# Kernel tuning notes

Measured on AMD Instinct MI355X. Metric: run time of the kernel, lower is better.

The kernel has to match this reference:

```python
import jax, jax.numpy as jnp
import numpy as np

GROUPS = 32
EPS = 1e-5


def setup_inputs() -> dict:
    key = jax.random.key(0)
    ks = jax.random.split(key, 7)
    B, C, H, W = 16, 512, 32, 32
    return {
        "x": jax.random.normal(ks[0], (B, C, H, W), jnp.float32),
        "norm_w": jax.random.uniform(ks[1], (C,), jnp.float32, 0.5, 1.5),
        "norm_b": jax.random.normal(ks[2], (C,), jnp.float32) * 0.1,
        "qkv_w": jax.random.normal(ks[3], (3 * C, C), jnp.float32) * (C ** -0.5),
        "qkv_b": jax.random.normal(ks[4], (3 * C,), jnp.float32) * 0.01,
        "proj_w": jax.random.normal(ks[5], (C, C), jnp.float32) * (C ** -0.5),
        "proj_b": jax.random.normal(ks[6], (C,), jnp.float32) * 0.01,
        "num_heads": 8,
    }


def _group_norm(x, w, b):
    # x: (B, C, T); GroupNorm over (C//G, T) per group, per-channel affine
    B, C, T = x.shape
    xg = x.reshape(B, GROUPS, C // GROUPS, T)
    mean = jnp.mean(xg, axis=(2, 3), keepdims=True)
    var = jnp.var(xg, axis=(2, 3), keepdims=True)
    xn = ((xg - mean) * jax.lax.rsqrt(var + EPS)).reshape(B, C, T)
    return xn * w[None, :, None] + b[None, :, None]


def reference(x, norm_w, norm_b, qkv_w, qkv_b, proj_w, proj_b, num_heads):
    B, C, H, W = x.shape
    T = H * W
    xf = x.reshape(B, C, T)
    # qkv conv1x1: (B, 3C, T)
    qkv = jnp.einsum('oc,bct->bot', qkv_w, _group_norm(xf, norm_w, norm_b)) \
        + qkv_b[None, :, None]
    # split heads: (B*H, 3*hd, T) then chunk on channel dim
    BH = B * num_heads
    qkv = qkv.reshape(BH, 3 * C // num_heads, T)
    q, k, v = jnp.split(qkv, 3, axis=1)  # each (BH, hd, T)
    hd = C // num_heads
    scale = hd ** -0.25
    # scores (BH, T, T), softmax in fp32 then cast back (matches torch)
    scores = jnp.einsum('bct,bcs->bts', q * scale, k * scale)
    w = jax.nn.softmax(scores.astype(jnp.float32), axis=-1).astype(scores.dtype)
    h = jnp.einsum('bts,bcs->bct', w, v)  # (BH, hd, T)
    h = h.reshape(B, C, T)
    h = jnp.einsum('oc,bct->bot', proj_w, h) + proj_b[None, :, None]
    return (h + xf).reshape(B, C, H, W)
```

## Files before the change

kernel.cpp:

```cpp
#include <hip/hip_runtime.h>

typedef unsigned short u16;
typedef unsigned int u32;
typedef __bf16 bf16x8 __attribute__((ext_vector_type(8)));
typedef float f32x4 __attribute__((ext_vector_type(4)));
typedef float f32x16 __attribute__((ext_vector_type(16)));

#define SCALE_QK 0.35355339059327373f
#define LOG2E 1.4426950408889634f

__device__ __forceinline__ u16 f2bf(float f) {
  u32 u = __float_as_uint(f);
  u += 0x7FFFu + ((u >> 16) & 1u);
  return (u16)(u >> 16);
}

__device__ __forceinline__ void gload16(const u16* g, u16* l) {
  __builtin_amdgcn_global_load_lds((const __attribute__((address_space(1))) void*)g,
                                   (__attribute__((address_space(3))) void*)l, 16, 0, 0);
}

__device__ __forceinline__ int rswz(int r) { return (r & 7) ^ ((r >> 3) & 3); }

__global__ __launch_bounds__(256) void k_convert(const float* __restrict__ src,
                                                 u16* __restrict__ dst, int n4) {
  int i = blockIdx.x * 256 + threadIdx.x;
  if (i >= n4) return;
  float4 v = ((const float4*)src)[i];
  u32 lo = (u32)f2bf(v.x) | ((u32)f2bf(v.y) << 16);
  u32 hi = (u32)f2bf(v.z) | ((u32)f2bf(v.w) << 16);
  ((uint2*)dst)[i] = make_uint2(lo, hi);
}

__global__ __launch_bounds__(256) void k_groupnorm(const float* __restrict__ x,
                                                   const float* __restrict__ nw,
                                                   const float* __restrict__ nb,
                                                   u16* __restrict__ gnt) {
  const int b = blockIdx.x >> 5;
  const int g = blockIdx.x & 31;
  const int tid = threadIdx.x;
  const float* xg = x + ((size_t)b * 512 + g * 16) * 1024;

  float s = 0.f, ss = 0.f;
#pragma unroll
  for (int it = 0; it < 16; ++it) {
    float4 v = ((const float4*)xg)[tid + it * 256];
    s += v.x + v.y + v.z + v.w;
    ss += v.x * v.x + v.y * v.y + v.z * v.z + v.w * v.w;
  }
#pragma unroll
  for (int off = 32; off >= 1; off >>= 1) {
    s += __shfl_xor(s, off);
    ss += __shfl_xor(ss, off);
  }
  __shared__ float red[8];
  const int wid = tid >> 6, lane = tid & 63;
  if (lane == 0) { red[wid] = s; red[4 + wid] = ss; }
  __syncthreads();
  const float mean = (red[0] + red[1] + red[2] + red[3]) * (1.f / 16384.f);
  const float ex2 = (red[4] + red[5] + red[6] + red[7]) * (1.f / 16384.f);
  const float rstd = rsqrtf(ex2 - mean * mean + 1e-5f);

  const int ci = tid & 15, tt = tid >> 4;
  const int c = g * 16 + ci;
  const float wc = nw[c] * rstd;
  const float bc = nb[c] - mean * wc;
  const float* xc = xg + (size_t)ci * 1024;
  u16* dst = gnt + (size_t)b * 1024 * 512 + c;
#pragma unroll 8
  for (int t = tt; t < 1024; t += 16) {
    dst[(size_t)t * 512] = f2bf(xc[t] * wc + bc);
  }
}

template <int MODE>
__global__ __launch_bounds__(512) void k_gemm(const u16* __restrict__ A,
                                              const u16* __restrict__ Bw,
                                              const float* __restrict__ bias,
                                              u16* __restrict__ Qb, u16* __restrict__ Kb,
                                              u16* __restrict__ Vb,
                                              const float* __restrict__ xres,
                                              float* __restrict__ out) {
  __shared__ u16 As[2][128][64];
  __shared__ u16 Bs[2][128][64];
  const int tid = threadIdx.x;
  const int lane = tid & 63, wid = tid >> 6;
  const int wr = wid >> 1, wc = wid & 1;
  const int fid = blockIdx.x;
  const int m0 = (fid & 127) * 128;
  const int n0 = (fid >> 7) * 128;
  const int l15 = lane & 15, l4 = lane >> 4;
  const f32x4 fzero = {0.f, 0.f, 0.f, 0.f};

  f32x4 acc[2][4];
#pragma unroll
  for (int i = 0; i < 2; ++i)
#pragma unroll
    for (int j = 0; j < 4; ++j) acc[i][j] = fzero;

  const int lrow = (tid & 63) >> 3;
  const int lchunk = tid & 7;

  auto stage = [&](int bi, int kt) {
#pragma unroll
    for (int rd = 0; rd < 2; ++rd) {
      const int rbase = wid * 8 + rd * 64;
      const int r = rbase + lrow;
      const int q = lchunk ^ (r & 7);
      gload16(A + ((size_t)(m0 + r) * 512 + kt * 64 + q * 8), &As[bi][rbase][0]);
      gload16(Bw + ((size_t)(n0 + r) * 512 + kt * 64 + q * 8), &Bs[bi][rbase][0]);
    }
  };

  stage(0, 0);
  stage(1, 1);

  for (int kt = 0; kt < 8; ++kt) {
    if (kt < 7) {
      asm volatile("s_waitcnt vmcnt(4)" ::: "memory");
    } else {
      asm volatile("s_waitcnt vmcnt(0)" ::: "memory");
    }
    __builtin_amdgcn_s_barrier();
    const int buf = kt & 1;
#pragma unroll
    for (int ks = 0; ks < 2; ++ks) {
      bf16x8 af[2], bfr[4];
#pragma unroll
      for (int mi = 0; mi < 2; ++mi) {
        const int row = wr * 32 + mi * 16 + l15;
        af[mi] = *(const bf16x8*)&As[buf][row][(((ks << 2) + l4) ^ (row & 7)) << 3];
      }
#pragma unroll
      for (int ni = 0; ni < 4; ++ni) {
        const int row = wc * 64 + ni * 16 + l15;
        bfr[ni] = *(const bf16x8*)&Bs[buf][row][(((ks << 2) + l4) ^ (row & 7)) << 3];
      }
#pragma unroll
      for (int mi = 0; mi < 2; ++mi)
#pragma unroll
        for (int ni = 0; ni < 4; ++ni)
          acc[mi][ni] = __builtin_amdgcn_mfma_f32_16x16x32_bf16(af[mi], bfr[ni], acc[mi][ni], 0, 0, 0);
    }
    asm volatile("s_waitcnt lgkmcnt(0)" ::: "memory");
    __builtin_amdgcn_sched_barrier(0);
    __builtin_amdgcn_s_barrier();
    if (kt < 6) stage(buf, kt + 2);
  }

#pragma unroll
  for (int ni = 0; ni < 4; ++ni) {
    const int o = n0 + wc * 64 + ni * 16 + l15;
    const float bo = bias[o];
    if (MODE == 0) {
      const int h = o / 192;
      const int jo = o - h * 192;
      const int typ = jo >> 6;
      const int ci = jo & 63;
#pragma unroll
      for (int mi = 0; mi < 2; ++mi) {
        const int mrow = m0 + wr * 32 + mi * 16 + l4 * 4;
        const int b = mrow >> 10, t0 = mrow & 1023;
#pragma unroll
        for (int jj = 0; jj < 4; ++jj) {
          const float v = acc[mi][ni][jj] + bo;
          const int t = t0 + jj;
          if (typ == 0)
            Qb[(((size_t)(b * 8 + h) * 1024 + t) << 6) + ci] = f2bf(v * (SCALE_QK * LOG2E));
          else if (typ == 1)
            Kb[(((size_t)(b * 8 + h) * 1024 + t) << 6) + ci] = f2bf(v * SCALE_QK);
          else
            Vb[(((size_t)(b * 8 + h) * 64 + ci) << 10) + t] = f2bf(v);
        }
      }
    } else {
#pragma unroll
      for (int mi = 0; mi < 2; ++mi) {
        const int mrow = m0 + wr * 32 + mi * 16 + l4 * 4;
        const int b = mrow >> 10, t0 = mrow & 1023;
        const size_t base = ((size_t)b * 512 + o) * 1024 + t0;
        const float4 xr = *(const float4*)(xres + base);
        float4 ov;
        ov.x = acc[mi][ni][0] + bo + xr.x;
        ov.y = acc[mi][ni][1] + bo + xr.y;
        ov.z = acc[mi][ni][2] + bo + xr.z;
        ov.w = acc[mi][ni][3] + bo + xr.w;
        *(float4*)(out + base) = ov;
      }
    }
  }
}

__global__ __launch_bounds__(256) void k_attn(const u16* __restrict__ Qb,
                                              const u16* __restrict__ Kb,
                                              const u16* __restrict__ Vb,
                                              u16* __restrict__ ht) {
  __shared__ u16 Ks[2][64][64];
  __shared__ u16 Vs[2][64][64];
  const int tid = threadIdx.x;
  const int lane = tid & 63, wid = tid >> 6;
  const int l31 = lane & 31, hi = lane >> 5;
  const int fid = blockIdx.x;
  const int bh = fid & 127, qt = fid >> 7;
  const int b = bh >> 3, head = bh & 7;
  const int lrow = lane >> 3, lchunk = lane & 7;
  const int rsw = rswz(l31);

  bf16x8 qf[4];
  {
    const u16* qp = Qb + (((size_t)bh * 1024 + qt * 128 + wid * 32 + l31) << 6) + hi * 8;
#pragma unroll
    for (int kc = 0; kc < 4; ++kc) qf[kc] = *(const bf16x8*)(qp + kc * 16);
  }

  bf16x8 onesf;
#pragma unroll
  for (int i = 0; i < 8; ++i) onesf[i] = (l31 == 0) ? (__bf16)1.0f : (__bf16)0.0f;

  f32x16 oacc[2], osum;
#pragma unroll
  for (int r = 0; r < 16; ++r) { oacc[0][r] = 0.f; oacc[1][r] = 0.f; osum[r] = 0.f; }

  auto stageKV = [&](int bi, int st) {
    const int s0 = st * 64;
#pragma unroll
    for (int rd = 0; rd < 2; ++rd) {
      const int rbase = wid * 8 + rd * 32;
      const int r = rbase + lrow;
      const int q = lchunk ^ rswz(r);
      gload16(Kb + (((size_t)bh * 1024 + s0 + r) << 6) + q * 8, &Ks[bi][rbase][0]);
      gload16(Vb + (((size_t)bh * 64 + r) << 10) + s0 + q * 8, &Vs[bi][rbase][0]);
    }
  };

  stageKV(0, 0);
  stageKV(1, 1);

  for (int st = 0; st < 16; ++st) {
    if (st < 15) {
      asm volatile("s_waitcnt vmcnt(4)" ::: "memory");
    } else {
      asm volatile("s_waitcnt vmcnt(0)" ::: "memory");
    }
    __builtin_amdgcn_s_barrier();
    const int buf = st & 1;

#pragma unroll
    for (int cb = 0; cb < 2; ++cb) {
      f32x16 sacc;
#pragma unroll
      for (int r = 0; r < 16; ++r) sacc[r] = 0.f;
      __builtin_amdgcn_s_setprio(1);
#pragma unroll
      for (int kc = 0; kc < 4; ++kc) {
        const int r = cb * 32 + l31;
        const bf16x8 kb = *(const bf16x8*)&Ks[buf][r][((((kc << 1) | hi)) ^ rsw) << 3];
        sacc = __builtin_amdgcn_mfma_f32_32x32x16_bf16(kb, qf[kc], sacc, 0, 0, 0);
      }
      __builtin_amdgcn_s_setprio(0);
      float p[16];
#pragma unroll
      for (int r = 0; r < 16; ++r)
        asm("v_exp_f32 %0, %1" : "=v"(p[r]) : "v"(sacc[r]));

#pragma unroll
      for (int ksl = 0; ksl < 2; ++ksl) {
        u32 X0, X1, Y0, Y1;
        asm("v_cvt_pk_bf16_f32 %0, %1, %2" : "=v"(X0) : "v"(p[8 * ksl + 0]), "v"(p[8 * ksl + 1]));
        asm("v_cvt_pk_bf16_f32 %0, %1, %2" : "=v"(X1) : "v"(p[8 * ksl + 2]), "v"(p[8 * ksl + 3]));
        asm("v_cvt_pk_bf16_f32 %0, %1, %2" : "=v"(Y0) : "v"(p[8 * ksl + 4]), "v"(p[8 * ksl + 5]));
        asm("v_cvt_pk_bf16_f32 %0, %1, %2" : "=v"(Y1) : "v"(p[8 * ksl + 6]), "v"(p[8 * ksl + 7]));
        asm volatile("v_permlane32_swap_b32 %0, %1" : "+v"(X0), "+v"(Y0));
        asm volatile("v_permlane32_swap_b32 %0, %1" : "+v"(X1), "+v"(Y1));
        union { u32 w[4]; bf16x8 v; } pa;
        pa.w[0] = X0; pa.w[1] = X1; pa.w[2] = Y0; pa.w[3] = Y1;
        const int ks = cb * 2 + ksl;
        __builtin_amdgcn_s_setprio(1);
#pragma unroll
        for (int db = 0; db < 2; ++db) {
          const int r = db * 32 + l31;
          const bf16x8 vb = *(const bf16x8*)&Vs[buf][r][((((ks << 1) | hi)) ^ rsw) << 3];
          oacc[db] = __builtin_amdgcn_mfma_f32_32x32x16_bf16(pa.v, vb, oacc[db], 0, 0, 0);
        }
        osum = __builtin_amdgcn_mfma_f32_32x32x16_bf16(pa.v, onesf, osum, 0, 0, 0);
        __builtin_amdgcn_s_setprio(0);
      }
    }

    asm volatile("s_waitcnt lgkmcnt(0)" ::: "memory");
    __builtin_amdgcn_sched_barrier(0);
    __builtin_amdgcn_s_barrier();
    if (st < 14) stageKV(buf, st + 2);
  }

  float inv[16];
#pragma unroll
  for (int r = 0; r < 16; ++r) {
    const float ls = __shfl(osum[r], lane & 32);
    inv[r] = 1.f / ls;
  }
#pragma unroll
  for (int db = 0; db < 2; ++db) {
#pragma unroll
    for (int r = 0; r < 16; ++r) {
      const int t = qt * 128 + wid * 32 + (r & 3) + 8 * (r >> 2) + 4 * hi;
      const int cg = head * 64 + db * 32 + l31;
      ht[((size_t)b * 1024 + t) * 512 + cg] = f2bf(oacc[db][r] * inv[r]);
    }
  }
}

extern "C" void kernel_launch(void* const* d_in, const int* in_sizes, int n_in,
                              void* d_out, int out_size, void* d_ws, size_t ws_size,
                              hipStream_t stream) {
  const float* x = (const float*)d_in[0];
  const float* norm_w = (const float*)d_in[1];
  const float* norm_b = (const float*)d_in[2];
  const float* qkv_w = (const float*)d_in[3];
  const float* qkv_b = (const float*)d_in[4];
  const float* proj_w = (const float*)d_in[5];
  const float* proj_b = (const float*)d_in[6];
  float* out = (float*)d_out;

  char* ws = (char*)d_ws;
  u16* qkvw = (u16*)(ws + 0);
  u16* projw = (u16*)(ws + 1572864);
  u16* gnt = (u16*)(ws + 2097152);
  u16* Qb = (u16*)(ws + 18874368);
  u16* Kb = (u16*)(ws + 35651584);
  u16* Vb = (u16*)(ws + 52428800);
  u16* ht = (u16*)(ws + 69206016);

  k_convert<<<768, 256, 0, stream>>>(qkv_w, qkvw, 196608);
  k_convert<<<256, 256, 0, stream>>>(proj_w, projw, 65536);
  k_groupnorm<<<512, 256, 0, stream>>>(x, norm_w, norm_b, gnt);
  k_gemm<0><<<1536, 512, 0, stream>>>(gnt, qkvw, qkv_b, Qb, Kb, Vb, nullptr, nullptr);
  k_attn<<<1024, 256, 0, stream>>>(Qb, Kb, Vb, ht);
  k_gemm<1><<<512, 512, 0, stream>>>(ht, projw, proj_b, nullptr, nullptr, nullptr, x, out);
}
```

Measured before the change: 154.5 us.

## Use 32x32 MFMA tiles in GEMMs and two query tiles per attention wave

```diff
diff --git a/kernel.cpp b/kernel.cpp
--- a/kernel.cpp
+++ b/kernel.cpp
@@ -74,7 +74,7 @@
 }
 
 template <int MODE>
-__global__ __launch_bounds__(512) void k_gemm(const u16* __restrict__ A,
+__global__ __launch_bounds__(256) void k_gemm(const u16* __restrict__ A,
                                               const u16* __restrict__ Bw,
                                               const float* __restrict__ bias,
                                               u16* __restrict__ Qb, u16* __restrict__ Kb,
@@ -85,30 +85,32 @@
   __shared__ u16 Bs[2][128][64];
   const int tid = threadIdx.x;
   const int lane = tid & 63, wid = tid >> 6;
-  const int wr = wid >> 1, wc = wid & 1;
+  const int wm = wid >> 1, wn = wid & 1;
   const int fid = blockIdx.x;
   const int m0 = (fid & 127) * 128;
   const int n0 = (fid >> 7) * 128;
-  const int l15 = lane & 15, l4 = lane >> 4;
-  const f32x4 fzero = {0.f, 0.f, 0.f, 0.f};
-
-  f32x4 acc[2][4];
+  const int l31 = lane & 31, hi = lane >> 5;
+  const int rsw = rswz(l31);
+
+  f32x16 acc[2][2];
 #pragma unroll
   for (int i = 0; i < 2; ++i)
 #pragma unroll
-    for (int j = 0; j < 4; ++j) acc[i][j] = fzero;
-
-  const int lrow = (tid & 63) >> 3;
-  const int lchunk = tid & 7;
+    for (int j = 0; j < 2; ++j)
+#pragma unroll
+      for (int r = 0; r < 16; ++r) acc[i][j][r] = 0.f;
+
+  const int lr8 = lane >> 3, lc8 = lane & 7;
 
   auto stage = [&](int bi, int kt) {
-#pragma unroll
-    for (int rd = 0; rd < 2; ++rd) {
-      const int rbase = wid * 8 + rd * 64;
-      const int r = rbase + lrow;
-      const int q = lchunk ^ (r & 7);
-      gload16(A + ((size_t)(m0 + r) * 512 + kt * 64 + q * 8), &As[bi][rbase][0]);
-      gload16(Bw + ((size_t)(n0 + r) * 512 + kt * 64 + q * 8), &Bs[bi][rbase][0]);
+    u16* ab = &As[bi][0][0] + wid * 512;
+    u16* bb = &Bs[bi][0][0] + wid * 512;
+#pragma unroll
+    for (int i = 0; i < 4; ++i) {
+      const int r = wid * 8 + i * 32 + lr8;
+      const int c8 = lc8 ^ rswz(r);
+      gload16(A + ((size_t)(m0 + r) * 512 + kt * 64 + c8 * 8), ab + i * 2048);
+      gload16(Bw + ((size_t)(n0 + r) * 512 + kt * 64 + c8 * 8), bb + i * 2048);
     }
   };
 
@@ -117,30 +119,31 @@
 
   for (int kt = 0; kt < 8; ++kt) {
     if (kt < 7) {
-      asm volatile("s_waitcnt vmcnt(4)" ::: "memory");
+      asm volatile("s_waitcnt vmcnt(8)" ::: "memory");
     } else {
       asm volatile("s_waitcnt vmcnt(0)" ::: "memory");
     }
     __builtin_amdgcn_s_barrier();
     const int buf = kt & 1;
 #pragma unroll
-    for (int ks = 0; ks < 2; ++ks) {
-      bf16x8 af[2], bfr[4];
+    for (int kc = 0; kc < 4; ++kc) {
+      const int ch = kc * 2 + hi;
+      bf16x8 af[2], bfv[2];
 #pragma unroll
       for (int mi = 0; mi < 2; ++mi) {
-        const int row = wr * 32 + mi * 16 + l15;
-        af[mi] = *(const bf16x8*)&As[buf][row][(((ks << 2) + l4) ^ (row & 7)) << 3];
-      }
-#pragma unroll
-      for (int ni = 0; ni < 4; ++ni) {
-        const int row = wc * 64 + ni * 16 + l15;
-        bfr[ni] = *(const bf16x8*)&Bs[buf][row][(((ks << 2) + l4) ^ (row & 7)) << 3];
+        const int row = wm * 64 + mi * 32 + l31;
+        af[mi] = *(const bf16x8*)&As[buf][row][(ch ^ rsw) << 3];
+      }
+#pragma unroll
+      for (int ni = 0; ni < 2; ++ni) {
+        const int row = wn * 64 + ni * 32 + l31;
+        bfv[ni] = *(const bf16x8*)&Bs[buf][row][(ch ^ rsw) << 3];
       }
 #pragma unroll
       for (int mi = 0; mi < 2; ++mi)
 #pragma unroll
-        for (int ni = 0; ni < 4; ++ni)
-          acc[mi][ni] = __builtin_amdgcn_mfma_f32_16x16x32_bf16(af[mi], bfr[ni], acc[mi][ni], 0, 0, 0);
+        for (int ni = 0; ni < 2; ++ni)
+          acc[mi][ni] = __builtin_amdgcn_mfma_f32_32x32x16_bf16(af[mi], bfv[ni], acc[mi][ni], 0, 0, 0);
     }
     asm volatile("s_waitcnt lgkmcnt(0)" ::: "memory");
     __builtin_amdgcn_sched_barrier(0);
@@ -148,44 +151,50 @@
     if (kt < 6) stage(buf, kt + 2);
   }
 
-#pragma unroll
-  for (int ni = 0; ni < 4; ++ni) {
-    const int o = n0 + wc * 64 + ni * 16 + l15;
+  const int b = m0 >> 10;
+  const int t0b = m0 & 1023;
+#pragma unroll
+  for (int ni = 0; ni < 2; ++ni) {
+    const int o = n0 + wn * 64 + ni * 32 + l31;
     const float bo = bias[o];
     if (MODE == 0) {
       const int h = o / 192;
       const int jo = o - h * 192;
       const int typ = jo >> 6;
       const int ci = jo & 63;
+      const size_t qkbase = ((size_t)(b * 8 + h) * 1024) * 64 + ci;
+      const size_t vbase = ((size_t)(b * 8 + h) * 64 + ci) * 1024;
 #pragma unroll
       for (int mi = 0; mi < 2; ++mi) {
-        const int mrow = m0 + wr * 32 + mi * 16 + l4 * 4;
-        const int b = mrow >> 10, t0 = mrow & 1023;
-#pragma unroll
-        for (int jj = 0; jj < 4; ++jj) {
-          const float v = acc[mi][ni][jj] + bo;
-          const int t = t0 + jj;
+        const int t0m = t0b + wm * 64 + mi * 32;
+#pragma unroll
+        for (int r = 0; r < 16; ++r) {
+          const int t = t0m + (r & 3) + 8 * (r >> 2) + 4 * hi;
+          const float v = acc[mi][ni][r] + bo;
           if (typ == 0)
-            Qb[(((size_t)(b * 8 + h) * 1024 + t) << 6) + ci] = f2bf(v * (SCALE_QK * LOG2E));
+            Qb[qkbase + (size_t)t * 64] = f2bf(v * (SCALE_QK * LOG2E));
           else if (typ == 1)
-            Kb[(((size_t)(b * 8 + h) * 1024 + t) << 6) + ci] = f2bf(v * SCALE_QK);
+            Kb[qkbase + (size_t)t * 64] = f2bf(v * SCALE_QK);
           else
-            Vb[(((size_t)(b * 8 + h) * 64 + ci) << 10) + t] = f2bf(v);
+            Vb[vbase + t] = f2bf(v);
         }
       }
     } else {
+      const size_t obase = ((size_t)b * 512 + o) * 1024;
 #pragma unroll
       for (int mi = 0; mi < 2; ++mi) {
-        const int mrow = m0 + wr * 32 + mi * 16 + l4 * 4;
-        const int b = mrow >> 10, t0 = mrow & 1023;
-        const size_t base = ((size_t)b * 512 + o) * 1024 + t0;
-        const float4 xr = *(const float4*)(xres + base);
-        float4 ov;
-        ov.x = acc[mi][ni][0] + bo + xr.x;
-        ov.y = acc[mi][ni][1] + bo + xr.y;
-        ov.z = acc[mi][ni][2] + bo + xr.z;
-        ov.w = acc[mi][ni][3] + bo + xr.w;
-        *(float4*)(out + base) = ov;
+        const int t0m = t0b + wm * 64 + mi * 32;
+#pragma unroll
+        for (int rq = 0; rq < 4; ++rq) {
+          const int t = t0m + 8 * rq + 4 * hi;
+          const float4 xr = *(const float4*)(xres + obase + t);
+          float4 ov;
+          ov.x = acc[mi][ni][rq * 4 + 0] + bo + xr.x;
+          ov.y = acc[mi][ni][rq * 4 + 1] + bo + xr.y;
+          ov.z = acc[mi][ni][rq * 4 + 2] + bo + xr.z;
+          ov.w = acc[mi][ni][rq * 4 + 3] + bo + xr.w;
+          *(float4*)(out + obase + t) = ov;
+        }
       }
     }
   }
@@ -206,20 +215,26 @@
   const int lrow = lane >> 3, lchunk = lane & 7;
   const int rsw = rswz(l31);
 
-  bf16x8 qf[4];
+  bf16x8 qf0[4], qf1[4];
   {
-    const u16* qp = Qb + (((size_t)bh * 1024 + qt * 128 + wid * 32 + l31) << 6) + hi * 8;
-#pragma unroll
-    for (int kc = 0; kc < 4; ++kc) qf[kc] = *(const bf16x8*)(qp + kc * 16);
+    const u16* qp0 = Qb + (((size_t)bh * 1024 + qt * 256 + wid * 64 + l31) << 6) + hi * 8;
+    const u16* qp1 = qp0 + (32 << 6);
+#pragma unroll
+    for (int kc = 0; kc < 4; ++kc) {
+      qf0[kc] = *(const bf16x8*)(qp0 + kc * 16);
+      qf1[kc] = *(const bf16x8*)(qp1 + kc * 16);
+    }
   }
 
   bf16x8 onesf;
 #pragma unroll
   for (int i = 0; i < 8; ++i) onesf[i] = (l31 == 0) ? (__bf16)1.0f : (__bf16)0.0f;
 
-  f32x16 oacc[2], osum;
-#pragma unroll
-  for (int r = 0; r < 16; ++r) { oacc[0][r] = 0.f; oacc[1][r] = 0.f; osum[r] = 0.f; }
+  f32x16 oacc[2][2], osum[2];
+#pragma unroll
+  for (int g = 0; g < 2; ++g)
+#pragma unroll
+    for (int r = 0; r < 16; ++r) { oacc[g][0][r] = 0.f; oacc[g][1][r] = 0.f; osum[g][r] = 0.f; }
 
   auto stageKV = [&](int bi, int st) {
     const int s0 = st * 64;
@@ -247,42 +262,54 @@
 
 #pragma unroll
     for (int cb = 0; cb < 2; ++cb) {
-      f32x16 sacc;
-#pragma unroll
-      for (int r = 0; r < 16; ++r) sacc[r] = 0.f;
+      f32x16 sacc0, sacc1;
+#pragma unroll
+      for (int r = 0; r < 16; ++r) { sacc0[r] = 0.f; sacc1[r] = 0.f; }
       __builtin_amdgcn_s_setprio(1);
 #pragma unroll
       for (int kc = 0; kc < 4; ++kc) {
         const int r = cb * 32 + l31;
         const bf16x8 kb = *(const bf16x8*)&Ks[buf][r][((((kc << 1) | hi)) ^ rsw) << 3];
-        sacc = __builtin_amdgcn_mfma_f32_32x32x16_bf16(kb, qf[kc], sacc, 0, 0, 0);
+        sacc0 = __builtin_amdgcn_mfma_f32_32x32x16_bf16(kb, qf0[kc], sacc0, 0, 0, 0);
+        sacc1 = __builtin_amdgcn_mfma_f32_32x32x16_bf16(kb, qf1[kc], sacc1, 0, 0, 0);
       }
       __builtin_amdgcn_s_setprio(0);
-      float p[16];
-#pragma unroll
-      for (int r = 0; r < 16; ++r)
-        asm("v_exp_f32 %0, %1" : "=v"(p[r]) : "v"(sacc[r]));
+      float p0[16], p1[16];
+#pragma unroll
+      for (int r = 0; r < 16; ++r) {
+        asm("v_exp_f32 %0, %1" : "=v"(p0[r]) : "v"(sacc0[r]));
+        asm("v_exp_f32 %0, %1" : "=v"(p1[r]) : "v"(sacc1[r]));
+      }
 
 #pragma unroll
       for (int ksl = 0; ksl < 2; ++ksl) {
-        u32 X0, X1, Y0, Y1;
-        asm("v_cvt_pk_bf16_f32 %0, %1, %2" : "=v"(X0) : "v"(p[8 * ksl + 0]), "v"(p[8 * ksl + 1]));
-        asm("v_cvt_pk_bf16_f32 %0, %1, %2" : "=v"(X1) : "v"(p[8 * ksl + 2]), "v"(p[8 * ksl + 3]));
-        asm("v_cvt_pk_bf16_f32 %0, %1, %2" : "=v"(Y0) : "v"(p[8 * ksl + 4]), "v"(p[8 * ksl + 5]));
-        asm("v_cvt_pk_bf16_f32 %0, %1, %2" : "=v"(Y1) : "v"(p[8 * ksl + 6]), "v"(p[8 * ksl + 7]));
-        asm volatile("v_permlane32_swap_b32 %0, %1" : "+v"(X0), "+v"(Y0));
-        asm volatile("v_permlane32_swap_b32 %0, %1" : "+v"(X1), "+v"(Y1));
-        union { u32 w[4]; bf16x8 v; } pa;
-        pa.w[0] = X0; pa.w[1] = X1; pa.w[2] = Y0; pa.w[3] = Y1;
+        u32 A0, A1, B0, B1, C0, C1, D0, D1;
+        asm("v_cvt_pk_bf16_f32 %0, %1, %2" : "=v"(A0) : "v"(p0[8 * ksl + 0]), "v"(p0[8 * ksl + 1]));
+        asm("v_cvt_pk_bf16_f32 %0, %1, %2" : "=v"(A1) : "v"(p0[8 * ksl + 2]), "v"(p0[8 * ksl + 3]));
+        asm("v_cvt_pk_bf16_f32 %0, %1, %2" : "=v"(B0) : "v"(p0[8 * ksl + 4]), "v"(p0[8 * ksl + 5]));
+        asm("v_cvt_pk_bf16_f32 %0, %1, %2" : "=v"(B1) : "v"(p0[8 * ksl + 6]), "v"(p0[8 * ksl + 7]));
+        asm volatile("v_permlane32_swap_b32 %0, %1" : "+v"(A0), "+v"(B0));
+        asm volatile("v_permlane32_swap_b32 %0, %1" : "+v"(A1), "+v"(B1));
+        asm("v_cvt_pk_bf16_f32 %0, %1, %2" : "=v"(C0) : "v"(p1[8 * ksl + 0]), "v"(p1[8 * ksl + 1]));
+        asm("v_cvt_pk_bf16_f32 %0, %1, %2" : "=v"(C1) : "v"(p1[8 * ksl + 2]), "v"(p1[8 * ksl + 3]));
+        asm("v_cvt_pk_bf16_f32 %0, %1, %2" : "=v"(D0) : "v"(p1[8 * ksl + 4]), "v"(p1[8 * ksl + 5]));
+        asm("v_cvt_pk_bf16_f32 %0, %1, %2" : "=v"(D1) : "v"(p1[8 * ksl + 6]), "v"(p1[8 * ksl + 7]));
+        asm volatile("v_permlane32_swap_b32 %0, %1" : "+v"(C0), "+v"(D0));
+        asm volatile("v_permlane32_swap_b32 %0, %1" : "+v"(C1), "+v"(D1));
+        union { u32 w[4]; bf16x8 v; } pa0, pa1;
+        pa0.w[0] = A0; pa0.w[1] = A1; pa0.w[2] = B0; pa0.w[3] = B1;
+        pa1.w[0] = C0; pa1.w[1] = C1; pa1.w[2] = D0; pa1.w[3] = D1;
         const int ks = cb * 2 + ksl;
         __builtin_amdgcn_s_setprio(1);
 #pragma unroll
         for (int db = 0; db < 2; ++db) {
           const int r = db * 32 + l31;
           const bf16x8 vb = *(const bf16x8*)&Vs[buf][r][((((ks << 1) | hi)) ^ rsw) << 3];
-          oacc[db] = __builtin_amdgcn_mfma_f32_32x32x16_bf16(pa.v, vb, oacc[db], 0, 0, 0);
+          oacc[0][db] = __builtin_amdgcn_mfma_f32_32x32x16_bf16(pa0.v, vb, oacc[0][db], 0, 0, 0);
+          oacc[1][db] = __builtin_amdgcn_mfma_f32_32x32x16_bf16(pa1.v, vb, oacc[1][db], 0, 0, 0);
         }
-        osum = __builtin_amdgcn_mfma_f32_32x32x16_bf16(pa.v, onesf, osum, 0, 0, 0);
+        osum[0] = __builtin_amdgcn_mfma_f32_32x32x16_bf16(pa0.v, onesf, osum[0], 0, 0, 0);
+        osum[1] = __builtin_amdgcn_mfma_f32_32x32x16_bf16(pa1.v, onesf, osum[1], 0, 0, 0);
         __builtin_amdgcn_s_setprio(0);
       }
     }
@@ -293,19 +320,23 @@
     if (st < 14) stageKV(buf, st + 2);
   }
 
-  float inv[16];
-#pragma unroll
-  for (int r = 0; r < 16; ++r) {
-    const float ls = __shfl(osum[r], lane & 32);
-    inv[r] = 1.f / ls;
-  }
-#pragma unroll
-  for (int db = 0; db < 2; ++db) {
+#pragma unroll
+  for (int g = 0; g < 2; ++g) {
+    float inv[16];
 #pragma unroll
     for (int r = 0; r < 16; ++r) {
-      const int t = qt * 128 + wid * 32 + (r & 3) + 8 * (r >> 2) + 4 * hi;
-      const int cg = head * 64 + db * 32 + l31;
-      ht[((size_t)b * 1024 + t) * 512 + cg] = f2bf(oacc[db][r] * inv[r]);
+      const float ls = __shfl(osum[g][r], lane & 32);
+      inv[r] = 1.f / ls;
+    }
+    const int tg = qt * 256 + wid * 64 + g * 32;
+#pragma unroll
+    for (int db = 0; db < 2; ++db) {
+#pragma unroll
+      for (int r = 0; r < 16; ++r) {
+        const int t = tg + (r & 3) + 8 * (r >> 2) + 4 * hi;
+        const int cg = head * 64 + db * 32 + l31;
+        ht[((size_t)b * 1024 + t) * 512 + cg] = f2bf(oacc[g][db][r] * inv[r]);
+      }
     }
   }
 }
@@ -334,7 +365,7 @@
   k_convert<<<768, 256, 0, stream>>>(qkv_w, qkvw, 196608);
   k_convert<<<256, 256, 0, stream>>>(proj_w, projw, 65536);
   k_groupnorm<<<512, 256, 0, stream>>>(x, norm_w, norm_b, gnt);
-  k_gemm<0><<<1536, 512, 0, stream>>>(gnt, qkvw, qkv_b, Qb, Kb, Vb, nullptr, nullptr);
-  k_attn<<<1024, 256, 0, stream>>>(Qb, Kb, Vb, ht);
-  k_gemm<1><<<512, 512, 0, stream>>>(ht, projw, proj_b, nullptr, nullptr, nullptr, x, out);
-}
+  k_gemm<0><<<1536, 256, 0, stream>>>(gnt, qkvw, qkv_b, Qb, Kb, Vb, nullptr, nullptr);
+  k_attn<<<512, 256, 0, stream>>>(Qb, Kb, Vb, ht);
+  k_gemm<1><<<512, 256, 0, stream>>>(ht, projw, proj_b, nullptr, nullptr, nullptr, x, out);
+}
```

After: 158.4 us. +2.5%, slower.

## Process two query tiles per wave in attention to reuse K/V fragments

Applied to the files above, without the earlier changes.

```diff
diff --git a/kernel.cpp b/kernel.cpp
--- a/kernel.cpp
+++ b/kernel.cpp
@@ -191,7 +191,7 @@
   }
 }
 
-__global__ __launch_bounds__(256) void k_attn(const u16* __restrict__ Qb,
+__global__ __launch_bounds__(128) void k_attn(const u16* __restrict__ Qb,
                                               const u16* __restrict__ Kb,
                                               const u16* __restrict__ Vb,
                                               u16* __restrict__ ht) {
@@ -206,26 +206,32 @@
   const int lrow = lane >> 3, lchunk = lane & 7;
   const int rsw = rswz(l31);
 
-  bf16x8 qf[4];
+  bf16x8 qf0[4], qf1[4];
   {
-    const u16* qp = Qb + (((size_t)bh * 1024 + qt * 128 + wid * 32 + l31) << 6) + hi * 8;
-#pragma unroll
-    for (int kc = 0; kc < 4; ++kc) qf[kc] = *(const bf16x8*)(qp + kc * 16);
+    const u16* qp0 = Qb + (((size_t)bh * 1024 + qt * 128 + wid * 64 + l31) << 6) + hi * 8;
+    const u16* qp1 = qp0 + (32 << 6);
+#pragma unroll
+    for (int kc = 0; kc < 4; ++kc) {
+      qf0[kc] = *(const bf16x8*)(qp0 + kc * 16);
+      qf1[kc] = *(const bf16x8*)(qp1 + kc * 16);
+    }
   }
 
   bf16x8 onesf;
 #pragma unroll
   for (int i = 0; i < 8; ++i) onesf[i] = (l31 == 0) ? (__bf16)1.0f : (__bf16)0.0f;
 
-  f32x16 oacc[2], osum;
-#pragma unroll
-  for (int r = 0; r < 16; ++r) { oacc[0][r] = 0.f; oacc[1][r] = 0.f; osum[r] = 0.f; }
+  f32x16 oacc[2][2], osum[2];
+#pragma unroll
+  for (int g = 0; g < 2; ++g)
+#pragma unroll
+    for (int r = 0; r < 16; ++r) { oacc[g][0][r] = 0.f; oacc[g][1][r] = 0.f; osum[g][r] = 0.f; }
 
   auto stageKV = [&](int bi, int st) {
     const int s0 = st * 64;
 #pragma unroll
-    for (int rd = 0; rd < 2; ++rd) {
-      const int rbase = wid * 8 + rd * 32;
+    for (int rd = 0; rd < 4; ++rd) {
+      const int rbase = wid * 32 + rd * 8;
       const int r = rbase + lrow;
       const int q = lchunk ^ rswz(r);
       gload16(Kb + (((size_t)bh * 1024 + s0 + r) << 6) + q * 8, &Ks[bi][rbase][0]);
@@ -238,7 +244,7 @@
 
   for (int st = 0; st < 16; ++st) {
     if (st < 15) {
-      asm volatile("s_waitcnt vmcnt(4)" ::: "memory");
+      asm volatile("s_waitcnt vmcnt(8)" ::: "memory");
     } else {
       asm volatile("s_waitcnt vmcnt(0)" ::: "memory");
     }
@@ -247,42 +253,54 @@
 
 #pragma unroll
     for (int cb = 0; cb < 2; ++cb) {
-      f32x16 sacc;
-#pragma unroll
-      for (int r = 0; r < 16; ++r) sacc[r] = 0.f;
+      f32x16 sacc0, sacc1;
+#pragma unroll
+      for (int r = 0; r < 16; ++r) { sacc0[r] = 0.f; sacc1[r] = 0.f; }
       __builtin_amdgcn_s_setprio(1);
 #pragma unroll
       for (int kc = 0; kc < 4; ++kc) {
         const int r = cb * 32 + l31;
         const bf16x8 kb = *(const bf16x8*)&Ks[buf][r][((((kc << 1) | hi)) ^ rsw) << 3];
-        sacc = __builtin_amdgcn_mfma_f32_32x32x16_bf16(kb, qf[kc], sacc, 0, 0, 0);
+        sacc0 = __builtin_amdgcn_mfma_f32_32x32x16_bf16(kb, qf0[kc], sacc0, 0, 0, 0);
+        sacc1 = __builtin_amdgcn_mfma_f32_32x32x16_bf16(kb, qf1[kc], sacc1, 0, 0, 0);
       }
       __builtin_amdgcn_s_setprio(0);
-      float p[16];
-#pragma unroll
-      for (int r = 0; r < 16; ++r)
-        asm("v_exp_f32 %0, %1" : "=v"(p[r]) : "v"(sacc[r]));
+      float p0[16], p1[16];
+#pragma unroll
+      for (int r = 0; r < 16; ++r) {
+        asm("v_exp_f32 %0, %1" : "=v"(p0[r]) : "v"(sacc0[r]));
+        asm("v_exp_f32 %0, %1" : "=v"(p1[r]) : "v"(sacc1[r]));
+      }
 
 #pragma unroll
       for (int ksl = 0; ksl < 2; ++ksl) {
-        u32 X0, X1, Y0, Y1;
-        asm("v_cvt_pk_bf16_f32 %0, %1, %2" : "=v"(X0) : "v"(p[8 * ksl + 0]), "v"(p[8 * ksl + 1]));
-        asm("v_cvt_pk_bf16_f32 %0, %1, %2" : "=v"(X1) : "v"(p[8 * ksl + 2]), "v"(p[8 * ksl + 3]));
-        asm("v_cvt_pk_bf16_f32 %0, %1, %2" : "=v"(Y0) : "v"(p[8 * ksl + 4]), "v"(p[8 * ksl + 5]));
-        asm("v_cvt_pk_bf16_f32 %0, %1, %2" : "=v"(Y1) : "v"(p[8 * ksl + 6]), "v"(p[8 * ksl + 7]));
-        asm volatile("v_permlane32_swap_b32 %0, %1" : "+v"(X0), "+v"(Y0));
-        asm volatile("v_permlane32_swap_b32 %0, %1" : "+v"(X1), "+v"(Y1));
-        union { u32 w[4]; bf16x8 v; } pa;
-        pa.w[0] = X0; pa.w[1] = X1; pa.w[2] = Y0; pa.w[3] = Y1;
+        u32 A0, A1, B0, B1, C0, C1, D0, D1;
+        asm("v_cvt_pk_bf16_f32 %0, %1, %2" : "=v"(A0) : "v"(p0[8 * ksl + 0]), "v"(p0[8 * ksl + 1]));
+        asm("v_cvt_pk_bf16_f32 %0, %1, %2" : "=v"(A1) : "v"(p0[8 * ksl + 2]), "v"(p0[8 * ksl + 3]));
+        asm("v_cvt_pk_bf16_f32 %0, %1, %2" : "=v"(B0) : "v"(p0[8 * ksl + 4]), "v"(p0[8 * ksl + 5]));
+        asm("v_cvt_pk_bf16_f32 %0, %1, %2" : "=v"(B1) : "v"(p0[8 * ksl + 6]), "v"(p0[8 * ksl + 7]));
+        asm volatile("v_permlane32_swap_b32 %0, %1" : "+v"(A0), "+v"(B0));
+        asm volatile("v_permlane32_swap_b32 %0, %1" : "+v"(A1), "+v"(B1));
+        asm("v_cvt_pk_bf16_f32 %0, %1, %2" : "=v"(C0) : "v"(p1[8 * ksl + 0]), "v"(p1[8 * ksl + 1]));
+        asm("v_cvt_pk_bf16_f32 %0, %1, %2" : "=v"(C1) : "v"(p1[8 * ksl + 2]), "v"(p1[8 * ksl + 3]));
+        asm("v_cvt_pk_bf16_f32 %0, %1, %2" : "=v"(D0) : "v"(p1[8 * ksl + 4]), "v"(p1[8 * ksl + 5]));
+        asm("v_cvt_pk_bf16_f32 %0, %1, %2" : "=v"(D1) : "v"(p1[8 * ksl + 6]), "v"(p1[8 * ksl + 7]));
+        asm volatile("v_permlane32_swap_b32 %0, %1" : "+v"(C0), "+v"(D0));
+        asm volatile("v_permlane32_swap_b32 %0, %1" : "+v"(C1), "+v"(D1));
+        union { u32 w[4]; bf16x8 v; } pa0, pa1;
+        pa0.w[0] = A0; pa0.w[1] = A1; pa0.w[2] = B0; pa0.w[3] = B1;
+        pa1.w[0] = C0; pa1.w[1] = C1; pa1.w[2] = D0; pa1.w[3] = D1;
         const int ks = cb * 2 + ksl;
         __builtin_amdgcn_s_setprio(1);
 #pragma unroll
         for (int db = 0; db < 2; ++db) {
           const int r = db * 32 + l31;
           const bf16x8 vb = *(const bf16x8*)&Vs[buf][r][((((ks << 1) | hi)) ^ rsw) << 3];
-          oacc[db] = __builtin_amdgcn_mfma_f32_32x32x16_bf16(pa.v, vb, oacc[db], 0, 0, 0);
+          oacc[0][db] = __builtin_amdgcn_mfma_f32_32x32x16_bf16(pa0.v, vb, oacc[0][db], 0, 0, 0);
+          oacc[1][db] = __builtin_amdgcn_mfma_f32_32x32x16_bf16(pa1.v, vb, oacc[1][db], 0, 0, 0);
         }
-        osum = __builtin_amdgcn_mfma_f32_32x32x16_bf16(pa.v, onesf, osum, 0, 0, 0);
+        osum[0] = __builtin_amdgcn_mfma_f32_32x32x16_bf16(pa0.v, onesf, osum[0], 0, 0, 0);
+        osum[1] = __builtin_amdgcn_mfma_f32_32x32x16_bf16(pa1.v, onesf, osum[1], 0, 0, 0);
         __builtin_amdgcn_s_setprio(0);
       }
     }
@@ -293,19 +311,23 @@
     if (st < 14) stageKV(buf, st + 2);
   }
 
-  float inv[16];
-#pragma unroll
-  for (int r = 0; r < 16; ++r) {
-    const float ls = __shfl(osum[r], lane & 32);
-    inv[r] = 1.f / ls;
-  }
-#pragma unroll
-  for (int db = 0; db < 2; ++db) {
+#pragma unroll
+  for (int g = 0; g < 2; ++g) {
+    float inv[16];
 #pragma unroll
     for (int r = 0; r < 16; ++r) {
-      const int t = qt * 128 + wid * 32 + (r & 3) + 8 * (r >> 2) + 4 * hi;
-      const int cg = head * 64 + db * 32 + l31;
-      ht[((size_t)b * 1024 + t) * 512 + cg] = f2bf(oacc[db][r] * inv[r]);
+      const float ls = __shfl(osum[g][r], lane & 32);
+      inv[r] = 1.f / ls;
+    }
+    const int tg = qt * 128 + wid * 64 + g * 32;
+#pragma unroll
+    for (int db = 0; db < 2; ++db) {
+#pragma unroll
+      for (int r = 0; r < 16; ++r) {
+        const int t = tg + (r & 3) + 8 * (r >> 2) + 4 * hi;
+        const int cg = head * 64 + db * 32 + l31;
+        ht[((size_t)b * 1024 + t) * 512 + cg] = f2bf(oacc[g][db][r] * inv[r]);
+      }
     }
   }
 }
@@ -335,6 +357,6 @@
   k_convert<<<256, 256, 0, stream>>>(proj_w, projw, 65536);
   k_groupnorm<<<512, 256, 0, stream>>>(x, norm_w, norm_b, gnt);
   k_gemm<0><<<1536, 512, 0, stream>>>(gnt, qkvw, qkv_b, Qb, Kb, Vb, nullptr, nullptr);
-  k_attn<<<1024, 256, 0, stream>>>(Qb, Kb, Vb, ht);
+  k_attn<<<1024, 128, 0, stream>>>(Qb, Kb, Vb, ht);
   k_gemm<1><<<512, 512, 0, stream>>>(ht, projw, proj_b, nullptr, nullptr, nullptr, x, out);
 }
```

Result: slower. 166.2 us (+7.6%).
